# Kernel tuning notes

Hardware: AMD Instinct MI355X
Metric: run time of the kernel (lower is better)

Reference implementation:

```python
import jax, jax.numpy as jnp
import numpy as np

DR = 0.1
L = 24.0
N_FRAMES = 16
N_ATOMS = 512


def setup_inputs() -> dict:
    key = jax.random.key(0)
    # coordinates uniform in the periodic box [0, L)^3
    traj = jax.random.uniform(key, (N_FRAMES, N_ATOMS, 3), dtype=jnp.float32) * L
    cell = jnp.eye(3, dtype=jnp.float32) * L
    # r_list = arange(0.5*dr, L_max - 2*dr, dr) with L_max = cell[0,0]/2 -> 118 bins
    r_list = jnp.arange(0.5 * DR, L / 2 - 2 * DR, DR, dtype=jnp.float32)
    return {"traj": traj, "cell": cell, "r_list": r_list}


def _frame_hist(q, cell_diag, r_list, cutoff_sq):
    # q: [N,3]; dense minimum-image pairwise displacements, upper-triangle pairs only
    disp = q[None, :, :] - q[:, None, :]                        # [N,N,3]
    offsets = jax.lax.stop_gradient(jnp.floor(disp / cell_diag + 0.5))
    disp = disp - offsets * cell_diag                           # minimum image
    sq = jnp.sum(disp * disp, axis=-1)                          # [N,N]
    n = q.shape[0]
    triu = jnp.triu(jnp.ones((n, n), dtype=bool))               # torch.triu zeros lower part
    sq = jnp.where(triu, sq, 0.0)
    mask = (sq < cutoff_sq) & (sq != 0.0)                       # i<j and within cutoff
    d = jnp.sqrt(jnp.where(mask, sq, 1.0))                      # safe sqrt (masked out below)
    centered = d[:, :, None] - r_list[None, None, :]            # [N,N,B]
    g = (1.0 / (DR * np.sqrt(2.0 * np.pi))) * jnp.exp(-0.5 * (centered / DR) ** 2)
    g = g * mask[:, :, None].astype(g.dtype)                    # drop excluded pairs (== nonzero extraction)
    return g.sum(axis=(0, 1)) * DR                              # [B]


def reference(traj, cell, r_list):
    cell_diag = jnp.diag(cell)                                  # [3]
    cutoff_sq = (cell[0, 0] / 2.0) ** 2                         # L_max = cell[0,0]/2 (default)

    def step(acc, q):
        return acc + _frame_hist(q, cell_diag, r_list, cutoff_sq), None

    hist0 = jnp.zeros(r_list.shape, dtype=traj.dtype)
    hist, _ = jax.lax.scan(step, hist0, traj)                   # accumulate over frames like the python loop
    hist = hist / traj.shape[0]

    v = (4.0 * np.pi / 3.0) * ((r_list + 0.5 * DR) ** 3 - (r_list - 0.5 * DR) ** 3)
    natom = traj.shape[1]
    det = jnp.linalg.det(cell)
    gr = hist / v * det / (natom - 1) / natom * 2.0
    return (r_list, gr)
```

## Files before the change

### kernel.cpp

```cpp
#include <hip/hip_runtime.h>
#include <math.h>

#define N_ATOMS 512
#define MAX_B 128
#define NBUCK 32
#define WIN 0.65f

__global__ void zero_kernel(float* p, int n) {
    int t = blockIdx.x * blockDim.x + threadIdx.x;
    if (t < n) p[t] = 0.0f;
}

__global__ __launch_bounds__(256) void pair_kernel(
    const float* __restrict__ traj, const float* __restrict__ cell,
    const float* __restrict__ r_list, float* __restrict__ part,
    int B, int atomic_mode)
{
    __shared__ float qx[N_ATOMS], qy[N_ATOMS], qz[N_ATOMS];
    __shared__ float dsorted[2048];
    __shared__ int   cnt[NBUCK];
    __shared__ int   start[NBUCK + 1];
    __shared__ int   cursor[NBUCK];
    __shared__ float accbuf[256];

    const int frame = blockIdx.x >> 6;
    const int sub   = blockIdx.x & 63;
    const int tid   = threadIdx.x;

    const float* q = traj + (size_t)frame * (N_ATOMS * 3);
    for (int a = tid; a < N_ATOMS; a += 256) {
        qx[a] = q[3 * a + 0];
        qy[a] = q[3 * a + 1];
        qz[a] = q[3 * a + 2];
    }
    if (tid < NBUCK) cnt[tid] = 0;
    __syncthreads();

    const float L = cell[0];
    const float invL = 1.0f / L;
    const float cutoff_sq = 0.25f * L * L;
    const float inv_bw = (float)NBUCK / (0.5f * L);

    float dval[8];
    int   dbuck[8];
    #pragma unroll
    for (int s = 0; s < 8; ++s) {
        const int qidx = s * 256 + tid;
        const int rp   = sub * 4 + (qidx >> 9);
        const int qq   = qidx & 511;
        const int lenA = 511 - rp;
        const bool inA = qq < lenA;
        const int i = inA ? rp : (510 - rp);
        const int j = inA ? (rp + 1 + qq) : qq;
        const bool vp = !(rp == 255 && !inA);

        float dx = qx[j] - qx[i];
        float dy = qy[j] - qy[i];
        float dz = qz[j] - qz[i];
        dx -= L * floorf(dx * invL + 0.5f);
        dy -= L * floorf(dy * invL + 0.5f);
        dz -= L * floorf(dz * invL + 0.5f);
        const float d2 = dx * dx + dy * dy + dz * dz;

        dbuck[s] = -1;
        dval[s]  = 0.0f;
        if (vp && d2 < cutoff_sq && d2 != 0.0f) {
            const float d = sqrtf(d2);
            int b = (int)(d * inv_bw);
            if (b > NBUCK - 1) b = NBUCK - 1;
            dval[s]  = d;
            dbuck[s] = b;
            atomicAdd(&cnt[b], 1);
        }
    }
    __syncthreads();

    if (tid < NBUCK) {
        const int v = cnt[tid];
        int incl = v;
        #pragma unroll
        for (int off = 1; off < NBUCK; off <<= 1) {
            const int n = __shfl_up(incl, off, 64);
            if (tid >= off) incl += n;
        }
        start[tid + 1] = incl;
        cursor[tid] = incl - v;
        if (tid == 0) start[0] = 0;
    }
    __syncthreads();

    #pragma unroll
    for (int s = 0; s < 8; ++s) {
        if (dbuck[s] >= 0) {
            const int pos = atomicAdd(&cursor[dbuck[s]], 1);
            dsorted[pos] = dval[s];
        }
    }
    __syncthreads();

    const int k = tid & 127;
    const int g = tid >> 7;
    float acc = 0.0f;
    if (k < B) {
        const float rk = r_list[k];
        const float c1 = -50.0f;
        const float c2 = 100.0f * rk;
        const float c3 = -50.0f * rk * rk;
        int blo = (int)(fmaxf((rk - WIN) * inv_bw, 0.0f));
        int bhi = (int)((rk + WIN) * inv_bw);
        if (bhi > NBUCK - 1) bhi = NBUCK - 1;
        const int lo = start[blo];
        const int hi = start[bhi + 1];
        for (int idx = lo + g; idx < hi; idx += 2) {
            const float d = dsorted[idx];
            acc += __expf(fmaf(d, fmaf(c1, d, c2), c3));
        }
    }
    accbuf[tid] = acc;
    __syncthreads();

    if (tid < 128) {
        const float v = accbuf[tid] + accbuf[tid + 128];
        if (atomic_mode) atomicAdd(&part[(blockIdx.x & 15) * MAX_B + tid], v);
        else             part[(size_t)blockIdx.x * MAX_B + tid] = v;
    }
}

__global__ __launch_bounds__(256) void finalize_kernel(
    const float* __restrict__ r_list, const float* __restrict__ cell,
    const float* __restrict__ part, float* __restrict__ out,
    int B, int F, int nrows)
{
    __shared__ float red[256];
    const int k = blockIdx.x;
    if (k >= B) return;

    float s = 0.0f;
    for (int t = threadIdx.x; t < nrows; t += 256) s += part[(size_t)t * MAX_B + k];
    red[threadIdx.x] = s;
    __syncthreads();
    for (int off = 128; off > 0; off >>= 1) {
        if (threadIdx.x < off) red[threadIdx.x] += red[threadIdx.x + off];
        __syncthreads();
    }
    if (threadIdx.x == 0) {
        const float r = r_list[k];
        out[k] = r;
        const float det = cell[0] * cell[4] * cell[8];
        const float rp = r + 0.05f;
        const float rm = r - 0.05f;
        const float v = (4.0f * (float)M_PI / 3.0f) * (rp * rp * rp - rm * rm * rm);
        const float inv_sqrt2pi = 0.3989422804014327f;
        const float h = red[0] * inv_sqrt2pi / (float)F;
        const float gr = h / v * det / (float)(N_ATOMS - 1) / (float)N_ATOMS * 2.0f;
        out[B + k] = gr;
    }
}

extern "C" void kernel_launch(void* const* d_in, const int* in_sizes, int n_in,
                              void* d_out, int out_size, void* d_ws, size_t ws_size,
                              hipStream_t stream) {
    const float* traj   = (const float*)d_in[0];
    const float* cell   = (const float*)d_in[1];
    const float* r_list = (const float*)d_in[2];
    float* out  = (float*)d_out;
    float* part = (float*)d_ws;

    const int B = in_sizes[2];
    const int F = in_sizes[0] / (N_ATOMS * 3);
    const int nblocks = F * 64;

    const bool partials_fit =
        ws_size >= (size_t)nblocks * MAX_B * sizeof(float);

    if (partials_fit) {
        hipLaunchKernelGGL(pair_kernel, dim3(nblocks), dim3(256), 0, stream,
                           traj, cell, r_list, part, B, 0);
        hipLaunchKernelGGL(finalize_kernel, dim3(MAX_B), dim3(256), 0, stream,
                           r_list, cell, part, out, B, F, nblocks);
    } else {
        hipLaunchKernelGGL(zero_kernel, dim3(8), dim3(256), 0, stream,
                           part, 16 * MAX_B);
        hipLaunchKernelGGL(pair_kernel, dim3(nblocks), dim3(256), 0, stream,
                           traj, cell, r_list, part, B, 1);
        hipLaunchKernelGGL(finalize_kernel, dim3(MAX_B), dim3(256), 0, stream,
                           r_list, cell, part, out, B, F, 16);
    }
}
```

Before: 76.69 us.

## Fuse pair histogram and finalize into one cooperative kernel with grid sync

Replaces the two-kernel path (pair kernel writing per-block partials, then a finalize kernel) with one cooperative launch. Blocks write transposed partials, wait at a grid-wide sync, and then the first B blocks each reduce one bin column and normalise it. This removes a kernel launch and its gap, at the cost of a grid-wide barrier across 1024 blocks, which must all be co-resident. The fallback atomic path is kept as a separate kernel, and its finalize now runs as a single small block.

```diff
diff --git a/kernel.cpp b/kernel.cpp
--- a/kernel.cpp
+++ b/kernel.cpp
@@ -1,20 +1,18 @@
 #include <hip/hip_runtime.h>
+#include <hip/hip_cooperative_groups.h>
 #include <math.h>
+
+namespace cg = cooperative_groups;
 
 #define N_ATOMS 512
 #define MAX_B 128
 #define NBUCK 32
 #define WIN 0.65f
 
-__global__ void zero_kernel(float* p, int n) {
-    int t = blockIdx.x * blockDim.x + threadIdx.x;
-    if (t < n) p[t] = 0.0f;
-}
-
-__global__ __launch_bounds__(256) void pair_kernel(
+__global__ __launch_bounds__(256) void rdf_fused(
     const float* __restrict__ traj, const float* __restrict__ cell,
     const float* __restrict__ r_list, float* __restrict__ part,
-    int B, int atomic_mode)
+    float* __restrict__ out, int B, int F, int nblocks)
 {
     __shared__ float qx[N_ATOMS], qy[N_ATOMS], qz[N_ATOMS];
     __shared__ float dsorted[2048];
@@ -66,11 +64,11 @@
         dval[s]  = 0.0f;
         if (vp && d2 < cutoff_sq && d2 != 0.0f) {
             const float d = sqrtf(d2);
-            int b = (int)(d * inv_bw);
-            if (b > NBUCK - 1) b = NBUCK - 1;
+            int bu = (int)(d * inv_bw);
+            if (bu > NBUCK - 1) bu = NBUCK - 1;
             dval[s]  = d;
-            dbuck[s] = b;
-            atomicAdd(&cnt[b], 1);
+            dbuck[s] = bu;
+            atomicAdd(&cnt[bu], 1);
         }
     }
     __syncthreads();
@@ -119,42 +117,151 @@
     accbuf[tid] = acc;
     __syncthreads();
 
-    if (tid < 128) {
-        const float v = accbuf[tid] + accbuf[tid + 128];
-        if (atomic_mode) atomicAdd(&part[(blockIdx.x & 15) * MAX_B + tid], v);
-        else             part[(size_t)blockIdx.x * MAX_B + tid] = v;
-    }
+    if (tid < MAX_B)
+        part[(size_t)tid * nblocks + blockIdx.x] = accbuf[tid] + accbuf[tid + 128];
+
+    cg::this_grid().sync();
+
+    const int b = blockIdx.x;
+    if (b < B) {
+        const float* col = part + (size_t)b * nblocks;
+        float s = 0.0f;
+        for (int t = tid; t < nblocks; t += 256) s += col[t];
+        accbuf[tid] = s;
+        __syncthreads();
+        #pragma unroll
+        for (int off = 128; off > 0; off >>= 1) {
+            if (tid < off) accbuf[tid] += accbuf[tid + off];
+            __syncthreads();
+        }
+        if (tid == 0) {
+            const float r = r_list[b];
+            out[b] = r;
+            const float det = cell[0] * cell[4] * cell[8];
+            const float rp = r + 0.05f;
+            const float rm = r - 0.05f;
+            const float v = (4.0f * (float)M_PI / 3.0f) * (rp * rp * rp - rm * rm * rm);
+            const float inv_sqrt2pi = 0.3989422804014327f;
+            const float h = accbuf[0] * inv_sqrt2pi / (float)F;
+            const float gr = h / v * det / (float)(N_ATOMS - 1) / (float)N_ATOMS * 2.0f;
+            out[B + b] = gr;
+        }
+    }
+}
+
+__global__ void zero_kernel(float* p, int n) {
+    int t = blockIdx.x * blockDim.x + threadIdx.x;
+    if (t < n) p[t] = 0.0f;
+}
+
+__global__ __launch_bounds__(256) void pair_kernel_atomic(
+    const float* __restrict__ traj, const float* __restrict__ cell,
+    const float* __restrict__ r_list, float* __restrict__ hist, int B)
+{
+    __shared__ float qx[N_ATOMS], qy[N_ATOMS], qz[N_ATOMS];
+    __shared__ float dsorted[2048];
+    __shared__ int   cnt[NBUCK];
+    __shared__ int   start[NBUCK + 1];
+    __shared__ int   cursor[NBUCK];
+    __shared__ float accbuf[256];
+
+    const int frame = blockIdx.x >> 6;
+    const int sub   = blockIdx.x & 63;
+    const int tid   = threadIdx.x;
+
+    const float* q = traj + (size_t)frame * (N_ATOMS * 3);
+    for (int a = tid; a < N_ATOMS; a += 256) {
+        qx[a] = q[3 * a + 0]; qy[a] = q[3 * a + 1]; qz[a] = q[3 * a + 2];
+    }
+    if (tid < NBUCK) cnt[tid] = 0;
+    __syncthreads();
+
+    const float L = cell[0];
+    const float invL = 1.0f / L;
+    const float cutoff_sq = 0.25f * L * L;
+    const float inv_bw = (float)NBUCK / (0.5f * L);
+
+    float dval[8]; int dbuck[8];
+    #pragma unroll
+    for (int s = 0; s < 8; ++s) {
+        const int qidx = s * 256 + tid;
+        const int rp   = sub * 4 + (qidx >> 9);
+        const int qq   = qidx & 511;
+        const bool inA = qq < (511 - rp);
+        const int i = inA ? rp : (510 - rp);
+        const int j = inA ? (rp + 1 + qq) : qq;
+        const bool vp = !(rp == 255 && !inA);
+        float dx = qx[j] - qx[i], dy = qy[j] - qy[i], dz = qz[j] - qz[i];
+        dx -= L * floorf(dx * invL + 0.5f);
+        dy -= L * floorf(dy * invL + 0.5f);
+        dz -= L * floorf(dz * invL + 0.5f);
+        const float d2 = dx * dx + dy * dy + dz * dz;
+        dbuck[s] = -1; dval[s] = 0.0f;
+        if (vp && d2 < cutoff_sq && d2 != 0.0f) {
+            const float d = sqrtf(d2);
+            int bu = (int)(d * inv_bw);
+            if (bu > NBUCK - 1) bu = NBUCK - 1;
+            dval[s] = d; dbuck[s] = bu;
+            atomicAdd(&cnt[bu], 1);
+        }
+    }
+    __syncthreads();
+    if (tid < NBUCK) {
+        const int v = cnt[tid];
+        int incl = v;
+        #pragma unroll
+        for (int off = 1; off < NBUCK; off <<= 1) {
+            const int n = __shfl_up(incl, off, 64);
+            if (tid >= off) incl += n;
+        }
+        start[tid + 1] = incl; cursor[tid] = incl - v;
+        if (tid == 0) start[0] = 0;
+    }
+    __syncthreads();
+    #pragma unroll
+    for (int s = 0; s < 8; ++s) {
+        if (dbuck[s] >= 0) {
+            const int pos = atomicAdd(&cursor[dbuck[s]], 1);
+            dsorted[pos] = dval[s];
+        }
+    }
+    __syncthreads();
+
+    const int k = tid & 127;
+    const int g = tid >> 7;
+    float acc = 0.0f;
+    if (k < B) {
+        const float rk = r_list[k];
+        const float c2 = 100.0f * rk, c3 = -50.0f * rk * rk;
+        int blo = (int)(fmaxf((rk - WIN) * inv_bw, 0.0f));
+        int bhi = (int)((rk + WIN) * inv_bw);
+        if (bhi > NBUCK - 1) bhi = NBUCK - 1;
+        for (int idx = start[blo] + g; idx < start[bhi + 1]; idx += 2) {
+            const float d = dsorted[idx];
+            acc += __expf(fmaf(d, fmaf(-50.0f, d, c2), c3));
+        }
+    }
+    accbuf[tid] = acc;
+    __syncthreads();
+    if (tid < MAX_B)
+        atomicAdd(&hist[(blockIdx.x & 15) * MAX_B + tid], accbuf[tid] + accbuf[tid + 128]);
 }
 
 __global__ __launch_bounds__(256) void finalize_kernel(
     const float* __restrict__ r_list, const float* __restrict__ cell,
-    const float* __restrict__ part, float* __restrict__ out,
-    int B, int F, int nrows)
+    const float* __restrict__ hist, float* __restrict__ out, int B, int F)
 {
-    __shared__ float red[256];
-    const int k = blockIdx.x;
+    const int k = blockIdx.x * blockDim.x + threadIdx.x;
     if (k >= B) return;
-
-    float s = 0.0f;
-    for (int t = threadIdx.x; t < nrows; t += 256) s += part[(size_t)t * MAX_B + k];
-    red[threadIdx.x] = s;
-    __syncthreads();
-    for (int off = 128; off > 0; off >>= 1) {
-        if (threadIdx.x < off) red[threadIdx.x] += red[threadIdx.x + off];
-        __syncthreads();
-    }
-    if (threadIdx.x == 0) {
-        const float r = r_list[k];
-        out[k] = r;
-        const float det = cell[0] * cell[4] * cell[8];
-        const float rp = r + 0.05f;
-        const float rm = r - 0.05f;
-        const float v = (4.0f * (float)M_PI / 3.0f) * (rp * rp * rp - rm * rm * rm);
-        const float inv_sqrt2pi = 0.3989422804014327f;
-        const float h = red[0] * inv_sqrt2pi / (float)F;
-        const float gr = h / v * det / (float)(N_ATOMS - 1) / (float)N_ATOMS * 2.0f;
-        out[B + k] = gr;
-    }
+    float h = 0.0f;
+    for (int rep = 0; rep < 16; ++rep) h += hist[rep * MAX_B + k];
+    const float r = r_list[k];
+    out[k] = r;
+    const float det = cell[0] * cell[4] * cell[8];
+    const float rp = r + 0.05f, rm = r - 0.05f;
+    const float v = (4.0f * (float)M_PI / 3.0f) * (rp * rp * rp - rm * rm * rm);
+    h = h * 0.3989422804014327f / (float)F;
+    out[B + k] = h / v * det / (float)(N_ATOMS - 1) / (float)N_ATOMS * 2.0f;
 }
 
 extern "C" void kernel_launch(void* const* d_in, const int* in_sizes, int n_in,
@@ -166,24 +273,20 @@
     float* out  = (float*)d_out;
     float* part = (float*)d_ws;
 
-    const int B = in_sizes[2];
-    const int F = in_sizes[0] / (N_ATOMS * 3);
-    const int nblocks = F * 64;
-
-    const bool partials_fit =
-        ws_size >= (size_t)nblocks * MAX_B * sizeof(float);
-
-    if (partials_fit) {
-        hipLaunchKernelGGL(pair_kernel, dim3(nblocks), dim3(256), 0, stream,
-                           traj, cell, r_list, part, B, 0);
-        hipLaunchKernelGGL(finalize_kernel, dim3(MAX_B), dim3(256), 0, stream,
-                           r_list, cell, part, out, B, F, nblocks);
+    int B = in_sizes[2];
+    int F = in_sizes[0] / (N_ATOMS * 3);
+    int nblocks = F * 64;
+
+    if (ws_size >= (size_t)MAX_B * nblocks * sizeof(float)) {
+        void* args[] = {&traj, &cell, &r_list, &part, &out, &B, &F, &nblocks};
+        hipLaunchCooperativeKernel((const void*)rdf_fused, dim3(nblocks), dim3(256),
+                                   args, 0, stream);
     } else {
         hipLaunchKernelGGL(zero_kernel, dim3(8), dim3(256), 0, stream,
                            part, 16 * MAX_B);
-        hipLaunchKernelGGL(pair_kernel, dim3(nblocks), dim3(256), 0, stream,
-                           traj, cell, r_list, part, B, 1);
-        hipLaunchKernelGGL(finalize_kernel, dim3(MAX_B), dim3(256), 0, stream,
-                           r_list, cell, part, out, B, F, 16);
-    }
-}
+        hipLaunchKernelGGL(pair_kernel_atomic, dim3(nblocks), dim3(256), 0, stream,
+                           traj, cell, r_list, part, B);
+        hipLaunchKernelGGL(finalize_kernel, dim3(1), dim3(MAX_B), 0, stream,
+                           r_list, cell, part, out, B, F);
+    }
+}
```

New measurement: 166.0 us. 116% more time.
